# Kernel tuning notes

Measured on AMD Instinct MI355X. Metric: run time of the kernel, lower is better.

## Reference

```python
import math
import jax, jax.numpy as jnp
import numpy as np

B, T, D = 4, 2048, 1024
H = 16
DK = D // H


def setup_inputs() -> dict:
    key = jax.random.key(0)
    ks = jax.random.split(key, 9)
    s = 1.0 / math.sqrt(D)
    return {
        "x": jax.random.normal(ks[0], (B, T, D), dtype=jnp.float32),
        "Wq": jax.random.normal(ks[1], (D, D), dtype=jnp.float32) * s,
        "bq": jax.random.normal(ks[2], (D,), dtype=jnp.float32) * s,
        "Wk": jax.random.normal(ks[3], (D, D), dtype=jnp.float32) * s,
        "bk": jax.random.normal(ks[4], (D,), dtype=jnp.float32) * s,
        "Wv": jax.random.normal(ks[5], (D, D), dtype=jnp.float32) * s,
        "bv": jax.random.normal(ks[6], (D,), dtype=jnp.float32) * s,
        "Wo": jax.random.normal(ks[7], (D, D), dtype=jnp.float32) * s,
        "bo": jax.random.normal(ks[8], (D,), dtype=jnp.float32) * s,
    }


def reference(x, Wq, bq, Wk, bk, Wv, bv, Wo, bo):
    Bx, Tx, C = x.shape
    # projections -> [B, H, T, d_k]
    q = (x @ Wq + bq).reshape(Bx, Tx, H, DK).transpose(0, 2, 1, 3)
    k = (x @ Wk + bk).reshape(Bx, Tx, H, DK).transpose(0, 2, 1, 3)
    v = (x @ Wv + bv).reshape(Bx, Tx, H, DK).transpose(0, 2, 1, 3)
    # scores [B, H, T, T], scaled
    scores = jnp.einsum("bhqd,bhkd->bhqk", q, k) / math.sqrt(DK)
    causal = jnp.tril(jnp.ones((Tx, Tx), dtype=bool))
    scores = jnp.where(causal[None, None, :, :], scores, -jnp.inf)
    attn = jax.nn.softmax(scores, axis=-1)  # dropout p=0.0 (eval)
    out = jnp.einsum("bhqk,bhkd->bhqd", attn, v)
    out = out.transpose(0, 2, 1, 3).reshape(Bx, Tx, C)
    return out @ Wo + bo
```

## Files before the change

kernel.cpp:

```cpp
#include <hip/hip_runtime.h>
#include <stdint.h>
#include <math.h>

typedef __attribute__((ext_vector_type(8))) __bf16 bf16x8;
typedef __attribute__((ext_vector_type(4))) float f32x4;

__device__ __forceinline__ void load_lds16(const void* g, void* l) {
  __builtin_amdgcn_global_load_lds((__attribute__((address_space(1))) void*)(g),
                                   (__attribute__((address_space(3))) void*)(l),
                                   16, 0, 0);
}

__global__ __launch_bounds__(256)
void convert_x(const float* __restrict__ xf, __bf16* __restrict__ xb) {
  const size_t i = ((size_t)blockIdx.x * 256 + threadIdx.x) * 8;
  const float4 u0 = *(const float4*)(xf + i);
  const float4 u1 = *(const float4*)(xf + i + 4);
  bf16x8 v;
  v[0] = (__bf16)u0.x; v[1] = (__bf16)u0.y; v[2] = (__bf16)u0.z; v[3] = (__bf16)u0.w;
  v[4] = (__bf16)u1.x; v[5] = (__bf16)u1.y; v[6] = (__bf16)u1.z; v[7] = (__bf16)u1.w;
  *(bf16x8*)&xb[i] = v;
}

__global__ __launch_bounds__(256)
void prep_weights(const float* __restrict__ Wq, const float* __restrict__ Wk,
                  const float* __restrict__ Wv, const float* __restrict__ Wo,
                  const float* __restrict__ bq, const float* __restrict__ bk,
                  const float* __restrict__ bv, const float* __restrict__ bo,
                  __bf16* __restrict__ Bt1, __bf16* __restrict__ Bt2,
                  float* __restrict__ bqkv, float* __restrict__ bo_f) {
  const int m = blockIdx.z;
  const float* W = (m == 0) ? Wq : (m == 1) ? Wk : (m == 2) ? Wv : Wo;
  __bf16* Out = (m == 3) ? Bt2 : Bt1 + (size_t)m * 1024 * 1024;
  const int kt = blockIdx.x * 64, nt = blockIdx.y * 64;
  __shared__ __bf16 tile[64 * 68];
  const int t = threadIdx.x;
#pragma unroll
  for (int i = 0; i < 16; i++) {
    int e = i * 256 + t;
    int r = e >> 6, c = e & 63;
    tile[r * 68 + c] = (__bf16)W[(size_t)(kt + r) * 1024 + nt + c];
  }
  __syncthreads();
#pragma unroll
  for (int i = 0; i < 16; i++) {
    int e = i * 256 + t;
    int r = e >> 6, c = e & 63;
    Out[(size_t)(nt + r) * 1024 + kt + c] = tile[c * 68 + r];
  }
  if (blockIdx.x == 0 && blockIdx.y == 0) {
    if (m < 3) {
      const float* bsrc = (m == 0) ? bq : (m == 1) ? bk : bv;
      for (int i = t; i < 1024; i += 256) bqkv[m * 1024 + i] = bsrc[i];
    } else {
      for (int i = t; i < 1024; i += 256) bo_f[i] = bo[i];
    }
  }
}

__global__ __launch_bounds__(256)
void gemm_bt(const __bf16* __restrict__ A, const __bf16* __restrict__ Bt,
             const float* __restrict__ bias, void* __restrict__ Cv,
             int out_f32, int M, int N, int K) {
  __shared__ __align__(16) __bf16 As[128 * 32];
  __shared__ __align__(16) __bf16 Bs[128 * 32];
  const int t = threadIdx.x;
  const int lane = t & 63;
  const int wave = t >> 6;
  const int bm = blockIdx.x * 128;
  const int bn = blockIdx.y * 128;
  const int wm = (wave >> 1) * 64;
  const int wn = (wave & 1) * 64;
  const int fm = lane & 15, fk = (lane >> 4) * 8;
  f32x4 acc[4][4] = {};

  const int r0 = t >> 2, kc = (t & 3) * 8;
  const __bf16* Ag0 = A + (size_t)(bm + r0) * K + kc;
  const __bf16* Ag1 = A + (size_t)(bm + 64 + r0) * K + kc;
  const __bf16* Bg0 = Bt + (size_t)(bn + r0) * K + kc;
  const __bf16* Bg1 = Bt + (size_t)(bn + 64 + r0) * K + kc;

  for (int k0 = 0; k0 < K; k0 += 32) {
    load_lds16(Ag0 + k0, &As[t * 8]);
    load_lds16(Ag1 + k0, &As[2048 + t * 8]);
    load_lds16(Bg0 + k0, &Bs[t * 8]);
    load_lds16(Bg1 + k0, &Bs[2048 + t * 8]);
    asm volatile("s_waitcnt vmcnt(0)" ::: "memory");
    __syncthreads();
    bf16x8 af[4], bfr[4];
#pragma unroll
    for (int i = 0; i < 4; i++) {
      af[i] = *(const bf16x8*)&As[(wm + i * 16 + fm) * 32 + fk];
      bfr[i] = *(const bf16x8*)&Bs[(wn + i * 16 + fm) * 32 + fk];
    }
#pragma unroll
    for (int i = 0; i < 4; i++)
#pragma unroll
      for (int j = 0; j < 4; j++)
        acc[i][j] = __builtin_amdgcn_mfma_f32_16x16x32_bf16(af[i], bfr[j], acc[i][j], 0, 0, 0);
    __syncthreads();
  }

  const int cm = (lane >> 4) * 4, cn = lane & 15;
#pragma unroll
  for (int i = 0; i < 4; i++)
#pragma unroll
    for (int j = 0; j < 4; j++) {
      const int col = bn + wn + j * 16 + cn;
      const float bvv = bias[col];
#pragma unroll
      for (int r = 0; r < 4; r++) {
        const int row = bm + wm + i * 16 + cm + r;
        const float val = acc[i][j][r] + bvv;
        if (out_f32) ((float*)Cv)[(size_t)row * N + col] = val;
        else ((__bf16*)Cv)[(size_t)row * N + col] = (__bf16)val;
      }
    }
}

__global__ __launch_bounds__(256)
void transpose_v(const __bf16* __restrict__ QKV, __bf16* __restrict__ Vt) {
  const int tt = blockIdx.x;
  const int bh = blockIdx.y;
  const int b = bh >> 4, h = bh & 15;
  __shared__ __bf16 tile[64 * 68];
  const int t = threadIdx.x;
#pragma unroll
  for (int i = 0; i < 16; i++) {
    int e = i * 256 + t;
    int tok = e >> 6, dk = e & 63;
    tile[tok * 68 + dk] =
        QKV[((size_t)b * 2048 + tt * 64 + tok) * 3072 + 2048 + h * 64 + dk];
  }
  __syncthreads();
#pragma unroll
  for (int i = 0; i < 16; i++) {
    int e = i * 256 + t;
    int dk = e >> 6, tok = e & 63;
    Vt[((size_t)bh * 64 + dk) * 2048 + tt * 64 + tok] = tile[tok * 68 + dk];
  }
}

__global__ __launch_bounds__(256)
void flash_attn(const __bf16* __restrict__ QKV, const __bf16* __restrict__ Vt,
                __bf16* __restrict__ O) {
  const int y = blockIdx.y;
  const int g = y >> 2, iy = y & 3;
  const int qt = (g == 0) ? (15 - 2 * iy)
               : (g == 1) ? (2 * iy)
               : (g == 2) ? (14 - 2 * iy)
                          : (2 * iy + 1);
  const int bh = blockIdx.x;
  const int b = bh >> 4, h = bh & 15;
  __shared__ __align__(16) __bf16 Ks[64 * 72];
  __shared__ __align__(16) __bf16 Vs[64 * 72];
  __shared__ __align__(16) __bf16 Ps[4 * 32 * 72];
  const int t = threadIdx.x, lane = t & 63, wave = t >> 6;
  const int fm = lane & 15, fq = lane >> 4;

  bf16x8 qf[2][2];
#pragma unroll
  for (int mi = 0; mi < 2; mi++) {
    const size_t qrow =
        ((size_t)b * 2048 + qt * 128 + wave * 32 + mi * 16 + fm) * 3072 + h * 64;
    qf[mi][0] = *(const bf16x8*)&QKV[qrow + fq * 8];
    qf[mi][1] = *(const bf16x8*)&QKV[qrow + 32 + fq * 8];
  }

  f32x4 o_acc[2][4] = {};
  float m_i[2][4], l_i[2][4];
#pragma unroll
  for (int mi = 0; mi < 2; mi++)
#pragma unroll
    for (int r = 0; r < 4; r++) { m_i[mi][r] = -1e30f; l_i[mi][r] = 0.f; }

  const int tok0 = t >> 3, ck = (t & 7) * 8;
  const size_t kbase = ((size_t)b * 2048) * 3072 + 1024 + h * 64;
  const size_t vbase = (size_t)bh * 64 * 2048;
  __bf16* Pw = &Ps[wave * 32 * 72];
  const int nkt = 2 * qt + 2;
  const int qmax_w = qt * 128 + wave * 32 + 31;
  const float SC = 0.18033688011112042f;

  bf16x8 pk0 = *(const bf16x8*)&QKV[kbase + (size_t)tok0 * 3072 + ck];
  bf16x8 pk1 = *(const bf16x8*)&QKV[kbase + (size_t)(32 + tok0) * 3072 + ck];
  bf16x8 pv0 = *(const bf16x8*)&Vt[vbase + (size_t)tok0 * 2048 + ck];
  bf16x8 pv1 = *(const bf16x8*)&Vt[vbase + (size_t)(32 + tok0) * 2048 + ck];

  for (int kt = 0; kt < nkt; kt++) {
    const int kb = kt * 64;
    __syncthreads();
    *(bf16x8*)&Ks[tok0 * 72 + ck] = pk0;
    *(bf16x8*)&Ks[(tok0 + 32) * 72 + ck] = pk1;
    *(bf16x8*)&Vs[tok0 * 72 + ck] = pv0;
    *(bf16x8*)&Vs[(tok0 + 32) * 72 + ck] = pv1;
    __syncthreads();

    if (kt + 1 < nkt) {
      const int kn = kb + 64;
      pk0 = *(const bf16x8*)&QKV[kbase + (size_t)(kn + tok0) * 3072 + ck];
      pk1 = *(const bf16x8*)&QKV[kbase + (size_t)(kn + 32 + tok0) * 3072 + ck];
      pv0 = *(const bf16x8*)&Vt[vbase + (size_t)tok0 * 2048 + kn + ck];
      pv1 = *(const bf16x8*)&Vt[vbase + (size_t)(32 + tok0) * 2048 + kn + ck];
    }

    if (kb > qmax_w) continue;

    f32x4 s[2][4];
#pragma unroll
    for (int nt = 0; nt < 4; nt++) {
      const bf16x8 kf0 = *(const bf16x8*)&Ks[(nt * 16 + fm) * 72 + fq * 8];
      const bf16x8 kf1 = *(const bf16x8*)&Ks[(nt * 16 + fm) * 72 + 32 + fq * 8];
#pragma unroll
      for (int mi = 0; mi < 2; mi++) {
        f32x4 z = {};
        z = __builtin_amdgcn_mfma_f32_16x16x32_bf16(qf[mi][0], kf0, z, 0, 0, 0);
        z = __builtin_amdgcn_mfma_f32_16x16x32_bf16(qf[mi][1], kf1, z, 0, 0, 0);
        s[mi][nt] = z;
      }
    }
    if (kt >= 2 * qt) {
#pragma unroll
      for (int mi = 0; mi < 2; mi++) {
        const int qg = qt * 128 + wave * 32 + mi * 16 + fq * 4;
#pragma unroll
        for (int nt = 0; nt < 4; nt++)
#pragma unroll
          for (int r = 0; r < 4; r++) {
            float v = s[mi][nt][r] * SC;
            if ((kb + nt * 16 + fm) > (qg + r)) v = -1e30f;
            s[mi][nt][r] = v;
          }
      }
    } else {
#pragma unroll
      for (int mi = 0; mi < 2; mi++)
#pragma unroll
        for (int nt = 0; nt < 4; nt++)
#pragma unroll
          for (int r = 0; r < 4; r++) s[mi][nt][r] *= SC;
    }

    float rmax[2][4], rsum[2][4], alpha[2][4];
#pragma unroll
    for (int mi = 0; mi < 2; mi++)
#pragma unroll
      for (int r = 0; r < 4; r++)
        rmax[mi][r] = fmaxf(fmaxf(s[mi][0][r], s[mi][1][r]),
                            fmaxf(s[mi][2][r], s[mi][3][r]));
#pragma unroll
    for (int off = 1; off < 16; off <<= 1)
#pragma unroll
      for (int mi = 0; mi < 2; mi++)
#pragma unroll
        for (int r = 0; r < 4; r++)
          rmax[mi][r] = fmaxf(rmax[mi][r], __shfl_xor(rmax[mi][r], off, 64));
#pragma unroll
    for (int mi = 0; mi < 2; mi++)
#pragma unroll
      for (int r = 0; r < 4; r++) {
        const float mn = fmaxf(m_i[mi][r], rmax[mi][r]);
        alpha[mi][r] = exp2f(m_i[mi][r] - mn);
        m_i[mi][r] = mn;
        rsum[mi][r] = 0.f;
      }
#pragma unroll
    for (int mi = 0; mi < 2; mi++)
#pragma unroll
      for (int nt = 0; nt < 4; nt++)
#pragma unroll
        for (int r = 0; r < 4; r++) {
          const float p = exp2f(s[mi][nt][r] - m_i[mi][r]);
          s[mi][nt][r] = p;
          rsum[mi][r] += p;
        }
#pragma unroll
    for (int off = 1; off < 16; off <<= 1)
#pragma unroll
      for (int mi = 0; mi < 2; mi++)
#pragma unroll
        for (int r = 0; r < 4; r++)
          rsum[mi][r] += __shfl_xor(rsum[mi][r], off, 64);
#pragma unroll
    for (int mi = 0; mi < 2; mi++)
#pragma unroll
      for (int r = 0; r < 4; r++)
        l_i[mi][r] = l_i[mi][r] * alpha[mi][r] + rsum[mi][r];

#pragma unroll
    for (int mi = 0; mi < 2; mi++)
#pragma unroll
      for (int nt = 0; nt < 4; nt++)
#pragma unroll
        for (int r = 0; r < 4; r++)
          Pw[(mi * 16 + fq * 4 + r) * 72 + nt * 16 + fm] = (__bf16)s[mi][nt][r];

    bf16x8 pf[2][2];
#pragma unroll
    for (int mi = 0; mi < 2; mi++) {
      pf[mi][0] = *(const bf16x8*)&Pw[(mi * 16 + fm) * 72 + fq * 8];
      pf[mi][1] = *(const bf16x8*)&Pw[(mi * 16 + fm) * 72 + 32 + fq * 8];
    }
#pragma unroll
    for (int dt = 0; dt < 4; dt++) {
      const bf16x8 vf0 = *(const bf16x8*)&Vs[(dt * 16 + fm) * 72 + fq * 8];
      const bf16x8 vf1 = *(const bf16x8*)&Vs[(dt * 16 + fm) * 72 + 32 + fq * 8];
#pragma unroll
      for (int mi = 0; mi < 2; mi++) {
        f32x4 o = o_acc[mi][dt];
#pragma unroll
        for (int r = 0; r < 4; r++) o[r] *= alpha[mi][r];
        o = __builtin_amdgcn_mfma_f32_16x16x32_bf16(pf[mi][0], vf0, o, 0, 0, 0);
        o = __builtin_amdgcn_mfma_f32_16x16x32_bf16(pf[mi][1], vf1, o, 0, 0, 0);
        o_acc[mi][dt] = o;
      }
    }
  }

#pragma unroll
  for (int mi = 0; mi < 2; mi++)
#pragma unroll
    for (int r = 0; r < 4; r++) l_i[mi][r] = 1.f / l_i[mi][r];
#pragma unroll
  for (int mi = 0; mi < 2; mi++) {
    const size_t orow = (size_t)b * 2048 + qt * 128 + wave * 32 + mi * 16 + fq * 4;
#pragma unroll
    for (int dt = 0; dt < 4; dt++)
#pragma unroll
      for (int r = 0; r < 4; r++)
        O[(orow + r) * 1024 + h * 64 + dt * 16 + fm] =
            (__bf16)(o_acc[mi][dt][r] * l_i[mi][r]);
  }
}

extern "C" void kernel_launch(void* const* d_in, const int* in_sizes, int n_in,
                              void* d_out, int out_size, void* d_ws, size_t ws_size,
                              hipStream_t stream) {
  const float* x = (const float*)d_in[0];
  const float* Wq = (const float*)d_in[1];
  const float* bq = (const float*)d_in[2];
  const float* Wk = (const float*)d_in[3];
  const float* bk = (const float*)d_in[4];
  const float* Wv = (const float*)d_in[5];
  const float* bv = (const float*)d_in[6];
  const float* Wo = (const float*)d_in[7];
  const float* bo = (const float*)d_in[8];

  char* ws = (char*)d_ws;
  __bf16* Bt1 = (__bf16*)(ws);
  __bf16* Bt2 = (__bf16*)(ws + 6291456);
  float* bqkv = (float*)(ws + 8388608);
  float* bo_f = (float*)(ws + 8400896);
  __bf16* QKV = (__bf16*)(ws + 8405504);
  __bf16* Vt = (__bf16*)(ws + 58737152);
  __bf16* Xb = (__bf16*)(ws + 75514368);
  __bf16* Ow = Xb;

  hipLaunchKernelGGL(convert_x, dim3(4096), dim3(256), 0, stream, x, Xb);
  hipLaunchKernelGGL(prep_weights, dim3(16, 16, 4), dim3(256), 0, stream,
                     Wq, Wk, Wv, Wo, bq, bk, bv, bo, Bt1, Bt2, bqkv, bo_f);
  hipLaunchKernelGGL(gemm_bt, dim3(64, 24), dim3(256), 0, stream,
                     Xb, Bt1, bqkv, (void*)QKV, 0, 8192, 3072, 1024);
  hipLaunchKernelGGL(transpose_v, dim3(32, 64), dim3(256), 0, stream, QKV, Vt);
  hipLaunchKernelGGL(flash_attn, dim3(64, 16), dim3(256), 0, stream, QKV, Vt, Ow);
  hipLaunchKernelGGL(gemm_bt, dim3(64, 8), dim3(256), 0, stream,
                     Ow, Bt2, bo_f, d_out, 1, 8192, 1024, 1024);
}
```

Measured before the change: 354.1 us.

## Enlarge attention blocks to 8 waves, add lazy rescaling and MFMA row sums

The flash attention kernel now uses 512-thread blocks covering 256 query rows, so each K/V tile loaded into shared memory serves twice as many queries, and each thread loads one K and one V vector per tile. The running-max rescale of the output accumulator and row sum is skipped unless some row's max grows by more than 8 in log2 units, and row sums are computed with an MFMA against a ones vector instead of shuffle reductions. These changes cut staging traffic, shuffle reductions and per-tile rescale work. In exchange there are fewer blocks to spread causal load imbalance across SMs, and the lazy threshold lets unnormalized probabilities grow up to 2^8 before the bf16 cast.

```diff
diff --git a/kernel.cpp b/kernel.cpp
--- a/kernel.cpp
+++ b/kernel.cpp
@@ -141,20 +141,16 @@
   }
 }
 
-__global__ __launch_bounds__(256)
+__global__ __launch_bounds__(512, 4)
 void flash_attn(const __bf16* __restrict__ QKV, const __bf16* __restrict__ Vt,
                 __bf16* __restrict__ O) {
-  const int y = blockIdx.y;
-  const int g = y >> 2, iy = y & 3;
-  const int qt = (g == 0) ? (15 - 2 * iy)
-               : (g == 1) ? (2 * iy)
-               : (g == 2) ? (14 - 2 * iy)
-                          : (2 * iy + 1);
+  const int qmap[8] = {7, 6, 5, 4, 0, 1, 2, 3};
+  const int qt = qmap[blockIdx.y];
   const int bh = blockIdx.x;
   const int b = bh >> 4, h = bh & 15;
   __shared__ __align__(16) __bf16 Ks[64 * 72];
   __shared__ __align__(16) __bf16 Vs[64 * 72];
-  __shared__ __align__(16) __bf16 Ps[4 * 32 * 72];
+  __shared__ __align__(16) __bf16 Ps[8 * 32 * 72];
   const int t = threadIdx.x, lane = t & 63, wave = t >> 6;
   const int fm = lane & 15, fq = lane >> 4;
 
@@ -162,7 +158,7 @@
 #pragma unroll
   for (int mi = 0; mi < 2; mi++) {
     const size_t qrow =
-        ((size_t)b * 2048 + qt * 128 + wave * 32 + mi * 16 + fm) * 3072 + h * 64;
+        ((size_t)b * 2048 + qt * 256 + wave * 32 + mi * 16 + fm) * 3072 + h * 64;
     qf[mi][0] = *(const bf16x8*)&QKV[qrow + fq * 8];
     qf[mi][1] = *(const bf16x8*)&QKV[qrow + 32 + fq * 8];
   }
@@ -178,30 +174,29 @@
   const size_t kbase = ((size_t)b * 2048) * 3072 + 1024 + h * 64;
   const size_t vbase = (size_t)bh * 64 * 2048;
   __bf16* Pw = &Ps[wave * 32 * 72];
-  const int nkt = 2 * qt + 2;
-  const int qmax_w = qt * 128 + wave * 32 + 31;
+  const int nkt = 4 * qt + 4;
+  const int qw = qt * 256 + wave * 32;
+  const int qmax_w = qw + 31;
   const float SC = 0.18033688011112042f;
 
-  bf16x8 pk0 = *(const bf16x8*)&QKV[kbase + (size_t)tok0 * 3072 + ck];
-  bf16x8 pk1 = *(const bf16x8*)&QKV[kbase + (size_t)(32 + tok0) * 3072 + ck];
-  bf16x8 pv0 = *(const bf16x8*)&Vt[vbase + (size_t)tok0 * 2048 + ck];
-  bf16x8 pv1 = *(const bf16x8*)&Vt[vbase + (size_t)(32 + tok0) * 2048 + ck];
+  bf16x8 ones;
+#pragma unroll
+  for (int i = 0; i < 8; i++) ones[i] = (__bf16)1.0f;
+
+  bf16x8 pk = *(const bf16x8*)&QKV[kbase + (size_t)tok0 * 3072 + ck];
+  bf16x8 pv = *(const bf16x8*)&Vt[vbase + (size_t)tok0 * 2048 + ck];
 
   for (int kt = 0; kt < nkt; kt++) {
     const int kb = kt * 64;
     __syncthreads();
-    *(bf16x8*)&Ks[tok0 * 72 + ck] = pk0;
-    *(bf16x8*)&Ks[(tok0 + 32) * 72 + ck] = pk1;
-    *(bf16x8*)&Vs[tok0 * 72 + ck] = pv0;
-    *(bf16x8*)&Vs[(tok0 + 32) * 72 + ck] = pv1;
+    *(bf16x8*)&Ks[tok0 * 72 + ck] = pk;
+    *(bf16x8*)&Vs[tok0 * 72 + ck] = pv;
     __syncthreads();
 
     if (kt + 1 < nkt) {
       const int kn = kb + 64;
-      pk0 = *(const bf16x8*)&QKV[kbase + (size_t)(kn + tok0) * 3072 + ck];
-      pk1 = *(const bf16x8*)&QKV[kbase + (size_t)(kn + 32 + tok0) * 3072 + ck];
-      pv0 = *(const bf16x8*)&Vt[vbase + (size_t)tok0 * 2048 + kn + ck];
-      pv1 = *(const bf16x8*)&Vt[vbase + (size_t)(32 + tok0) * 2048 + kn + ck];
+      pk = *(const bf16x8*)&QKV[kbase + (size_t)(kn + tok0) * 3072 + ck];
+      pv = *(const bf16x8*)&Vt[vbase + (size_t)tok0 * 2048 + kn + ck];
     }
 
     if (kb > qmax_w) continue;
@@ -219,10 +214,10 @@
         s[mi][nt] = z;
       }
     }
-    if (kt >= 2 * qt) {
+    if (kb + 63 > qw) {
 #pragma unroll
       for (int mi = 0; mi < 2; mi++) {
-        const int qg = qt * 128 + wave * 32 + mi * 16 + fq * 4;
+        const int qg = qw + mi * 16 + fq * 4;
 #pragma unroll
         for (int nt = 0; nt < 4; nt++)
 #pragma unroll
@@ -241,7 +236,7 @@
           for (int r = 0; r < 4; r++) s[mi][nt][r] *= SC;
     }
 
-    float rmax[2][4], rsum[2][4], alpha[2][4];
+    float rmax[2][4];
 #pragma unroll
     for (int mi = 0; mi < 2; mi++)
 #pragma unroll
@@ -255,45 +250,38 @@
 #pragma unroll
         for (int r = 0; r < 4; r++)
           rmax[mi][r] = fmaxf(rmax[mi][r], __shfl_xor(rmax[mi][r], off, 64));
+
+    float grow = -1e30f;
 #pragma unroll
     for (int mi = 0; mi < 2; mi++)
 #pragma unroll
-      for (int r = 0; r < 4; r++) {
-        const float mn = fmaxf(m_i[mi][r], rmax[mi][r]);
-        alpha[mi][r] = exp2f(m_i[mi][r] - mn);
-        m_i[mi][r] = mn;
-        rsum[mi][r] = 0.f;
-      }
+      for (int r = 0; r < 4; r++) grow = fmaxf(grow, rmax[mi][r] - m_i[mi][r]);
+    if (!__all(grow <= 8.0f)) {
+#pragma unroll
+      for (int mi = 0; mi < 2; mi++) {
+        float a[4];
+#pragma unroll
+        for (int r = 0; r < 4; r++) {
+          const float mn = fmaxf(m_i[mi][r], rmax[mi][r]);
+          a[r] = exp2f(m_i[mi][r] - mn);
+          m_i[mi][r] = mn;
+          l_i[mi][r] *= a[r];
+        }
+#pragma unroll
+        for (int dt = 0; dt < 4; dt++)
+#pragma unroll
+          for (int r = 0; r < 4; r++) o_acc[mi][dt][r] *= a[r];
+      }
+    }
+
 #pragma unroll
     for (int mi = 0; mi < 2; mi++)
 #pragma unroll
       for (int nt = 0; nt < 4; nt++)
 #pragma unroll
-        for (int r = 0; r < 4; r++) {
-          const float p = exp2f(s[mi][nt][r] - m_i[mi][r]);
-          s[mi][nt][r] = p;
-          rsum[mi][r] += p;
-        }
-#pragma unroll
-    for (int off = 1; off < 16; off <<= 1)
-#pragma unroll
-      for (int mi = 0; mi < 2; mi++)
-#pragma unroll
         for (int r = 0; r < 4; r++)
-          rsum[mi][r] += __shfl_xor(rsum[mi][r], off, 64);
-#pragma unroll
-    for (int mi = 0; mi < 2; mi++)
-#pragma unroll
-      for (int r = 0; r < 4; r++)
-        l_i[mi][r] = l_i[mi][r] * alpha[mi][r] + rsum[mi][r];
-
-#pragma unroll
-    for (int mi = 0; mi < 2; mi++)
-#pragma unroll
-      for (int nt = 0; nt < 4; nt++)
-#pragma unroll
-        for (int r = 0; r < 4; r++)
-          Pw[(mi * 16 + fq * 4 + r) * 72 + nt * 16 + fm] = (__bf16)s[mi][nt][r];
+          Pw[(mi * 16 + fq * 4 + r) * 72 + nt * 16 + fm] =
+              (__bf16)exp2f(s[mi][nt][r] - m_i[mi][r]);
 
     bf16x8 pf[2][2];
 #pragma unroll
@@ -301,6 +289,16 @@
       pf[mi][0] = *(const bf16x8*)&Pw[(mi * 16 + fm) * 72 + fq * 8];
       pf[mi][1] = *(const bf16x8*)&Pw[(mi * 16 + fm) * 72 + 32 + fq * 8];
     }
+
+#pragma unroll
+    for (int mi = 0; mi < 2; mi++) {
+      f32x4 rs = {};
+      rs = __builtin_amdgcn_mfma_f32_16x16x32_bf16(pf[mi][0], ones, rs, 0, 0, 0);
+      rs = __builtin_amdgcn_mfma_f32_16x16x32_bf16(pf[mi][1], ones, rs, 0, 0, 0);
+#pragma unroll
+      for (int r = 0; r < 4; r++) l_i[mi][r] += rs[r];
+    }
+
 #pragma unroll
     for (int dt = 0; dt < 4; dt++) {
       const bf16x8 vf0 = *(const bf16x8*)&Vs[(dt * 16 + fm) * 72 + fq * 8];
@@ -308,8 +306,6 @@
 #pragma unroll
       for (int mi = 0; mi < 2; mi++) {
         f32x4 o = o_acc[mi][dt];
-#pragma unroll
-        for (int r = 0; r < 4; r++) o[r] *= alpha[mi][r];
         o = __builtin_amdgcn_mfma_f32_16x16x32_bf16(pf[mi][0], vf0, o, 0, 0, 0);
         o = __builtin_amdgcn_mfma_f32_16x16x32_bf16(pf[mi][1], vf1, o, 0, 0, 0);
         o_acc[mi][dt] = o;
@@ -323,7 +319,7 @@
     for (int r = 0; r < 4; r++) l_i[mi][r] = 1.f / l_i[mi][r];
 #pragma unroll
   for (int mi = 0; mi < 2; mi++) {
-    const size_t orow = (size_t)b * 2048 + qt * 128 + wave * 32 + mi * 16 + fq * 4;
+    const size_t orow = (size_t)b * 2048 + qt * 256 + wave * 32 + mi * 16 + fq * 4;
 #pragma unroll
     for (int dt = 0; dt < 4; dt++)
 #pragma unroll
@@ -362,7 +358,7 @@
   hipLaunchKernelGGL(gemm_bt, dim3(64, 24), dim3(256), 0, stream,
                      Xb, Bt1, bqkv, (void*)QKV, 0, 8192, 3072, 1024);
   hipLaunchKernelGGL(transpose_v, dim3(32, 64), dim3(256), 0, stream, QKV, Vt);
-  hipLaunchKernelGGL(flash_attn, dim3(64, 16), dim3(256), 0, stream, QKV, Vt, Ow);
+  hipLaunchKernelGGL(flash_attn, dim3(64, 8), dim3(512), 0, stream, QKV, Vt, Ow);
   hipLaunchKernelGGL(gemm_bt, dim3(64, 8), dim3(256), 0, stream,
                      Ow, Bt2, bo_f, d_out, 1, 8192, 1024, 1024);
 }
```

Result: slower. 385.1 us (+8.7%).
